# Performance work log

Measured on AMD Instinct MI355X. Metric: run time of the kernel, lower is better.

## Reference

```python
import jax, jax.numpy as jnp
import numpy as np

D_MODEL = 1024
NHEAD = 16
D_K = D_MODEL // NHEAD
BATCH = 8
SEQ = 1024
SPARSITY = 0.9


def setup_inputs() -> dict:
    key = jax.random.key(0)
    ks = jax.random.split(key, 13)
    q = jax.random.normal(ks[0], (BATCH, SEQ, D_MODEL), dtype=jnp.float32)
    k = jax.random.normal(ks[1], (BATCH, SEQ, D_MODEL), dtype=jnp.float32)
    v = jax.random.normal(ks[2], (BATCH, SEQ, D_MODEL), dtype=jnp.float32)
    mask = jax.random.uniform(ks[3], (BATCH, NHEAD, SEQ, SEQ)) > SPARSITY
    s = 1.0 / np.sqrt(D_MODEL)  # nn.Linear-style init scale
    def lin(kw, kb):
        W = jax.random.uniform(kw, (D_MODEL, D_MODEL), minval=-s, maxval=s, dtype=jnp.float32)
        b = jax.random.uniform(kb, (D_MODEL,), minval=-s, maxval=s, dtype=jnp.float32)
        return W, b
    Wq, bq = lin(ks[4], ks[5])
    Wk, bk = lin(ks[6], ks[7])
    Wv, bv = lin(ks[8], ks[9])
    Wo, bo = lin(ks[10], ks[11])
    return {"query": q, "key": k, "value": v, "mask": mask,
            "Wq": Wq, "bq": bq, "Wk": Wk, "bk": bk,
            "Wv": Wv, "bv": bv, "Wo": Wo, "bo": bo}


def reference(query, key, value, mask, Wq, bq, Wk, bk, Wv, bv, Wo, bo):
    B, S, _ = query.shape
    # projections (torch Linear: x @ W.T + b), split into heads -> [B, H, S, d_k]
    def proj(x, W, b):
        return (x @ W.T + b).reshape(B, S, NHEAD, D_K).transpose(0, 2, 1, 3)
    Q = proj(query, Wq, bq)
    K = proj(key, Wk, bk)
    V = proj(value, Wv, bv)
    scale = 1.0 / jnp.sqrt(jnp.float32(D_K))
    scores = jnp.einsum('bhqd,bhkd->bhqk', Q, K) * scale  # [B,H,S,S]
    scores = jnp.where(mask, scores, -jnp.inf)
    attn = jax.nn.softmax(scores, axis=-1)
    out = jnp.einsum('bhqk,bhkd->bhqd', attn, V)           # [B,H,S,d_k]
    out = out.transpose(0, 2, 1, 3).reshape(B, S, D_MODEL)
    return out @ Wo.T + bo
```

## Files before the change

### kernel.cpp

```cpp
#include <hip/hip_runtime.h>

typedef __bf16 bf16;
typedef bf16 bf16x4 __attribute__((ext_vector_type(4)));
typedef bf16 bf16x8 __attribute__((ext_vector_type(8)));
typedef float f32x4 __attribute__((ext_vector_type(4)));

#define D_MODEL 1024
#define NHEAD   16
#define D_K     64
#define BATCH   8
#define SEQL    1024
#define MROWS   (BATCH*SEQL)

struct Cvt7 {
    const float* s[7];
    bf16*        d[7];
    int          n[7];
};

__global__ __launch_bounds__(256) void cvt7_kernel(Cvt7 a) {
    const int y = blockIdx.y;
    const float* __restrict__ src = a.s[y];
    bf16* __restrict__ dst = a.d[y];
    const int n4 = a.n[y] >> 2;
    const int stride = gridDim.x * blockDim.x;
    for (int i = blockIdx.x * blockDim.x + threadIdx.x; i < n4; i += stride) {
        float4 v = ((const float4*)src)[i];
        bf16x4 o = { (bf16)v.x, (bf16)v.y, (bf16)v.z, (bf16)v.w };
        ((bf16x4*)dst)[i] = o;
    }
}

#define BM 128
#define BN 128
#define BK 32

__device__ __forceinline__ void gemm_core(const bf16* __restrict__ A, const bf16* __restrict__ B,
                                          int bm, int bn, int K,
                                          bf16* lA, bf16* lB, f32x4 (&acc)[4][4]) {
    const int t = threadIdx.x;
    const int lane = t & 63, w = t >> 6;
    const int wr = w >> 1, wc = w & 1;
    const int r = lane & 15, kb = lane >> 4;

    for (int k0 = 0; k0 < K; k0 += BK) {
        __syncthreads();
        #pragma unroll
        for (int i = 0; i < 2; ++i) {
            const int off = i * 4096 + w * 1024 + lane * 16;
            const int row = off >> 6;
            const int cb  = off & 63;
            const bf16* srcA = A + (size_t)(bm + row) * K + k0 + (cb >> 1);
            const bf16* srcB = B + (size_t)(bn + row) * K + k0 + (cb >> 1);
            __builtin_amdgcn_global_load_lds(
                (const __attribute__((address_space(1))) unsigned int*)srcA,
                (__attribute__((address_space(3))) unsigned int*)((char*)lA + i * 4096 + w * 1024),
                16, 0, 0);
            __builtin_amdgcn_global_load_lds(
                (const __attribute__((address_space(1))) unsigned int*)srcB,
                (__attribute__((address_space(3))) unsigned int*)((char*)lB + i * 4096 + w * 1024),
                16, 0, 0);
        }
        __syncthreads();

        bf16x8 af[4], bfr[4];
        #pragma unroll
        for (int m = 0; m < 4; ++m)
            af[m] = *(const bf16x8*)(lA + (wr * 64 + m * 16 + r) * BK + kb * 8);
        #pragma unroll
        for (int n = 0; n < 4; ++n)
            bfr[n] = *(const bf16x8*)(lB + (wc * 64 + n * 16 + r) * BK + kb * 8);
        #pragma unroll
        for (int m = 0; m < 4; ++m)
            #pragma unroll
            for (int n = 0; n < 4; ++n)
                acc[m][n] = __builtin_amdgcn_mfma_f32_16x16x32_bf16(af[m], bfr[n], acc[m][n], 0, 0, 0);
    }
}

__global__ __launch_bounds__(256) void proj3_kernel(
        const bf16* __restrict__ xq, const bf16* __restrict__ xk, const bf16* __restrict__ xv,
        const bf16* __restrict__ Wqb, const bf16* __restrict__ Wkb, const bf16* __restrict__ Wvb,
        const float* __restrict__ bq, const float* __restrict__ bk, const float* __restrict__ bv,
        bf16* __restrict__ Qp, bf16* __restrict__ Kp, bf16* __restrict__ Vt) {
    __shared__ bf16 lA[BM * BK], lB[BN * BK];
    const int z = blockIdx.z;
    const bf16* A    = (z == 0) ? xq  : (z == 1) ? xk  : xv;
    const bf16* Bm   = (z == 0) ? Wqb : (z == 1) ? Wkb : Wvb;
    const float* bias = (z == 0) ? bq : (z == 1) ? bk  : bv;
    const int bm = blockIdx.x * BM, bn = blockIdx.y * BN;

    f32x4 acc[4][4] = {};
    gemm_core(A, Bm, bm, bn, D_MODEL, lA, lB, acc);

    const int lane = threadIdx.x & 63, w = threadIdx.x >> 6;
    const int wr = w >> 1, wc = w & 1, r = lane & 15, g = lane >> 4;
    #pragma unroll
    for (int n = 0; n < 4; ++n) {
        const int col = bn + wc * 64 + n * 16 + r;
        const float bvl = bias[col];
        const int h = col >> 6, d = col & 63;
        #pragma unroll
        for (int m = 0; m < 4; ++m) {
            #pragma unroll
            for (int j = 0; j < 4; ++j) {
                const int row = bm + wr * 64 + m * 16 + g * 4 + j;
                const float v = acc[m][n][j] + bvl;
                const int b = row >> 10, s = row & (SEQL - 1);
                const int bh = b * NHEAD + h;
                if (z == 0) {
                    Qp[((size_t)bh * SEQL + s) * D_K + d] = (bf16)v;
                } else if (z == 1) {
                    Kp[((size_t)bh * SEQL + s) * D_K + d] = (bf16)v;
                } else {
                    Vt[((size_t)bh * D_K + d) * SEQL + s] = (bf16)v;
                }
            }
        }
    }
}

__global__ __launch_bounds__(256) void outproj_kernel(
        const bf16* __restrict__ AO, const bf16* __restrict__ Wob,
        const float* __restrict__ bo, float* __restrict__ out) {
    __shared__ bf16 lA[BM * BK], lB[BN * BK];
    const int bm = blockIdx.x * BM, bn = blockIdx.y * BN;
    f32x4 acc[4][4] = {};
    gemm_core(AO, Wob, bm, bn, D_MODEL, lA, lB, acc);

    const int lane = threadIdx.x & 63, w = threadIdx.x >> 6;
    const int wr = w >> 1, wc = w & 1, r = lane & 15, g = lane >> 4;
    #pragma unroll
    for (int n = 0; n < 4; ++n) {
        const int col = bn + wc * 64 + n * 16 + r;
        const float bvl = bo[col];
        #pragma unroll
        for (int m = 0; m < 4; ++m)
            #pragma unroll
            for (int j = 0; j < 4; ++j) {
                const int row = bm + wr * 64 + m * 16 + g * 4 + j;
                out[(size_t)row * D_MODEL + col] = acc[m][n][j] + bvl;
            }
    }
}

__global__ __launch_bounds__(256, 4) void attn_kernel(
        const bf16* __restrict__ Qp, const bf16* __restrict__ Kp, const bf16* __restrict__ Vt,
        const unsigned int* __restrict__ mask, bf16* __restrict__ AO) {
    __shared__ char kbuf[8192];
    __shared__ char vbuf[8192];
    __shared__ char mbuf[16384];
    __shared__ bf16 plds[4][16 * 64];
    const int lin = blockIdx.x + blockIdx.y * gridDim.x;
    const int xcd = lin & 7, pos = lin >> 3;
    const int bh  = xcd * 16 + (pos >> 4);
    const int qt  = pos & 15;
    const int b = bh >> 4, h = bh & 15;
    const int t = threadIdx.x, lane = t & 63, w = t >> 6;
    const int q0 = qt * 64;
    const int r = lane & 15, g = lane >> 4;

    const char* __restrict__ Kb = (const char*)(Kp + (size_t)bh * SEQL * D_K);
    const char* __restrict__ Vb = (const char*)(Vt + (size_t)bh * D_K * SEQL);
    const char* __restrict__ Mb = (const char*)(mask + ((size_t)bh * SEQL + q0) * SEQL);

    const bf16* __restrict__ Qh = Qp + ((size_t)bh * SEQL + q0 + w * 16) * D_K;
    bf16x8 qf[2];
    #pragma unroll
    for (int kk = 0; kk < 2; ++kk)
        qf[kk] = *(const bf16x8*)(Qh + r * D_K + kk * 32 + g * 8);

    f32x4 o[4] = {};
    float psum = 0.f;
    char* P = (char*)plds[w];
    const int swz = (r & 7) << 4;

    for (int s0 = 0; s0 < SEQL; s0 += 64) {
        __syncthreads();
        #pragma unroll
        for (int i = 0; i < 2; ++i) {
            const int slot = i * 256 + t;
            const int row = slot >> 3, ch = slot & 7;
            const char* srcK = Kb + (size_t)(s0 + row) * 128 + ((ch * 16) ^ ((row & 7) << 4));
            const char* srcV = Vb + (size_t)row * (SEQL * 2) + s0 * 2 + ((ch * 16) ^ ((row & 7) << 4));
            __builtin_amdgcn_global_load_lds(
                (const __attribute__((address_space(1))) unsigned int*)srcK,
                (__attribute__((address_space(3))) unsigned int*)(kbuf + i * 4096 + w * 1024),
                16, 0, 0);
            __builtin_amdgcn_global_load_lds(
                (const __attribute__((address_space(1))) unsigned int*)srcV,
                (__attribute__((address_space(3))) unsigned int*)(vbuf + i * 4096 + w * 1024),
                16, 0, 0);
        }
        #pragma unroll
        for (int i = 0; i < 4; ++i) {
            const int slot = i * 256 + t;
            const int row = slot >> 4, ch = slot & 15;
            const char* srcM = Mb + (size_t)row * (SEQL * 4) + s0 * 4 + ((ch * 16) ^ ((row & 7) << 4));
            __builtin_amdgcn_global_load_lds(
                (const __attribute__((address_space(1))) unsigned int*)srcM,
                (__attribute__((address_space(3))) unsigned int*)(mbuf + i * 4096 + w * 1024),
                16, 0, 0);
        }
        __syncthreads();

        f32x4 sf[4] = {};
        __builtin_amdgcn_s_setprio(1);
        #pragma unroll
        for (int n = 0; n < 4; ++n) {
            #pragma unroll
            for (int kk = 0; kk < 2; ++kk) {
                const int krow = n * 16 + r;
                bf16x8 kf = *(const bf16x8*)(kbuf + krow * 128 + ((kk * 64 + g * 16) ^ swz));
                sf[n] = __builtin_amdgcn_mfma_f32_16x16x32_bf16(kf, qf[kk], sf[n], 0, 0, 0);
            }
        }
        __builtin_amdgcn_s_setprio(0);
        const int mrow = w * 16 + r;
        #pragma unroll
        for (int n = 0; n < 4; ++n) {
            const uint4 mv = *(const uint4*)(mbuf + mrow * 256 + ((n * 64 + g * 16) ^ swz));
            const float p0 = mv.x ? __expf(sf[n][0] * 0.125f) : 0.f;
            const float p1 = mv.y ? __expf(sf[n][1] * 0.125f) : 0.f;
            const float p2 = mv.z ? __expf(sf[n][2] * 0.125f) : 0.f;
            const float p3 = mv.w ? __expf(sf[n][3] * 0.125f) : 0.f;
            psum += (p0 + p1) + (p2 + p3);
            bf16x4 pb = { (bf16)p0, (bf16)p1, (bf16)p2, (bf16)p3 };
            *(bf16x4*)(P + ((r * 128 + n * 32 + g * 8) ^ swz)) = pb;
        }
        bf16x8 pf0 = *(const bf16x8*)(P + ((r * 128 + 0 * 64 + g * 16) ^ swz));
        bf16x8 pf1 = *(const bf16x8*)(P + ((r * 128 + 1 * 64 + g * 16) ^ swz));
        __builtin_amdgcn_s_setprio(1);
        #pragma unroll
        for (int n = 0; n < 4; ++n) {
            const int vrow = n * 16 + r;
            bf16x8 vf0 = *(const bf16x8*)(vbuf + vrow * 128 + ((0 * 64 + g * 16) ^ swz));
            bf16x8 vf1 = *(const bf16x8*)(vbuf + vrow * 128 + ((1 * 64 + g * 16) ^ swz));
            o[n] = __builtin_amdgcn_mfma_f32_16x16x32_bf16(vf0, pf0, o[n], 0, 0, 0);
            o[n] = __builtin_amdgcn_mfma_f32_16x16x32_bf16(vf1, pf1, o[n], 0, 0, 0);
        }
        __builtin_amdgcn_s_setprio(0);
    }

    psum += __shfl_xor(psum, 16);
    psum += __shfl_xor(psum, 32);
    const float inv = 1.0f / psum;

    const size_t rowbase = ((size_t)(b * SEQL + q0 + w * 16 + r)) * D_MODEL + h * D_K;
    #pragma unroll
    for (int n = 0; n < 4; ++n) {
        bf16x4 ob = { (bf16)(o[n][0] * inv), (bf16)(o[n][1] * inv),
                      (bf16)(o[n][2] * inv), (bf16)(o[n][3] * inv) };
        *(bf16x4*)(AO + rowbase + n * 16 + g * 4) = ob;
    }
}

extern "C" void kernel_launch(void* const* d_in, const int* in_sizes, int n_in,
                              void* d_out, int out_size, void* d_ws, size_t ws_size,
                              hipStream_t stream) {
    const float* q    = (const float*)d_in[0];
    const float* k    = (const float*)d_in[1];
    const float* v    = (const float*)d_in[2];
    const unsigned int* mask = (const unsigned int*)d_in[3];
    const float* Wq = (const float*)d_in[4];
    const float* bq = (const float*)d_in[5];
    const float* Wk = (const float*)d_in[6];
    const float* bk = (const float*)d_in[7];
    const float* Wv = (const float*)d_in[8];
    const float* bv = (const float*)d_in[9];
    const float* Wo = (const float*)d_in[10];
    const float* bo = (const float*)d_in[11];

    char* ws = (char*)d_ws;
    const size_t MB = 1u << 20;
    bf16* qb  = (bf16*)(ws + 0 * MB);
    bf16* kb  = (bf16*)(ws + 16 * MB);
    bf16* vb  = (bf16*)(ws + 32 * MB);
    bf16* Wqb = (bf16*)(ws + 48 * MB);
    bf16* Wkb = (bf16*)(ws + 50 * MB);
    bf16* Wvb = (bf16*)(ws + 52 * MB);
    bf16* Wob = (bf16*)(ws + 54 * MB);
    bf16* Qp  = (bf16*)(ws + 56 * MB);
    bf16* Kp  = (bf16*)(ws + 72 * MB);
    bf16* Vt  = (bf16*)(ws + 88 * MB);
    bf16* AO  = (bf16*)(ws + 104 * MB);

    Cvt7 c;
    c.s[0] = q;  c.d[0] = qb;  c.n[0] = MROWS * D_MODEL;
    c.s[1] = k;  c.d[1] = kb;  c.n[1] = MROWS * D_MODEL;
    c.s[2] = v;  c.d[2] = vb;  c.n[2] = MROWS * D_MODEL;
    c.s[3] = Wq; c.d[3] = Wqb; c.n[3] = D_MODEL * D_MODEL;
    c.s[4] = Wk; c.d[4] = Wkb; c.n[4] = D_MODEL * D_MODEL;
    c.s[5] = Wv; c.d[5] = Wvb; c.n[5] = D_MODEL * D_MODEL;
    c.s[6] = Wo; c.d[6] = Wob; c.n[6] = D_MODEL * D_MODEL;
    cvt7_kernel<<<dim3(1024, 7), 256, 0, stream>>>(c);

    proj3_kernel<<<dim3(MROWS / BM, D_MODEL / BN, 3), 256, 0, stream>>>(
        qb, kb, vb, Wqb, Wkb, Wvb, bq, bk, bv, Qp, Kp, Vt);

    attn_kernel<<<dim3(SEQL / 64, BATCH * NHEAD), 256, 0, stream>>>(Qp, Kp, Vt, mask, AO);

    outproj_kernel<<<dim3(MROWS / BM, D_MODEL / BN), 256, 0, stream>>>(AO, Wob, bo, (float*)d_out);
}
```

Measured before the change: 292.1 us.

## Pack mask into bitmask concurrently with projections; read bits in attention

Adds a mask-packing path that turns the 32-bit-per-element mask into 64-bit ballot bitmasks. It runs in every fourth block of the merged projection kernel, so it overlaps with the Q/K/V GEMMs. The attention kernel then loads each tile's packed mask bits once into LDS, instead of streaming the full uint mask per key tile, which cuts its mask traffic by a large factor. The full mask is still read once during packing, and the packed mask is stored temporarily in the output buffer before outproj overwrites it.

```diff
diff --git a/kernel.cpp b/kernel.cpp
--- a/kernel.cpp
+++ b/kernel.cpp
@@ -11,6 +11,7 @@
 #define BATCH   8
 #define SEQL    1024
 #define MROWS   (BATCH*SEQL)
+#define MWORDS  ((size_t)BATCH*NHEAD*SEQL*SEQL)
 
 struct Cvt7 {
     const float* s[7];
@@ -78,17 +79,41 @@
     }
 }
 
-__global__ __launch_bounds__(256) void proj3_kernel(
+__global__ __launch_bounds__(256) void projpack_kernel(
         const bf16* __restrict__ xq, const bf16* __restrict__ xk, const bf16* __restrict__ xv,
         const bf16* __restrict__ Wqb, const bf16* __restrict__ Wkb, const bf16* __restrict__ Wvb,
         const float* __restrict__ bq, const float* __restrict__ bk, const float* __restrict__ bv,
+        const unsigned int* __restrict__ mask, unsigned long long* __restrict__ Mp,
         bf16* __restrict__ Qp, bf16* __restrict__ Kp, bf16* __restrict__ Vt) {
     __shared__ bf16 lA[BM * BK], lB[BN * BK];
-    const int z = blockIdx.z;
+    const int bid = blockIdx.x;
+
+    if ((bid & 3) == 3) {
+        const int lane = threadIdx.x & 63;
+        const int wid  = (((bid >> 2) * 256 + threadIdx.x) >> 6);
+        const size_t ngrp = MWORDS / 256;
+        for (size_t i = wid; i < ngrp; i += 2048) {
+            const unsigned int* base = mask + i * 256;
+            const unsigned long long o0 = __ballot(base[0 * 64 + lane] != 0);
+            const unsigned long long o1 = __ballot(base[1 * 64 + lane] != 0);
+            const unsigned long long o2 = __ballot(base[2 * 64 + lane] != 0);
+            const unsigned long long o3 = __ballot(base[3 * 64 + lane] != 0);
+            if (lane < 4) {
+                const unsigned long long v = lane == 0 ? o0 : lane == 1 ? o1 : lane == 2 ? o2 : o3;
+                Mp[i * 4 + lane] = v;
+            }
+        }
+        return;
+    }
+
+    const int projIdx = (bid >> 2) * 3 + (bid & 3);
+    const int z   = projIdx / 512;
+    const int rem = projIdx % 512;
+    const int bm = (rem & 63) * BM;
+    const int bn = (rem >> 6) * BN;
     const bf16* A    = (z == 0) ? xq  : (z == 1) ? xk  : xv;
     const bf16* Bm   = (z == 0) ? Wqb : (z == 1) ? Wkb : Wvb;
     const float* bias = (z == 0) ? bq : (z == 1) ? bk  : bv;
-    const int bm = blockIdx.x * BM, bn = blockIdx.y * BN;
 
     f32x4 acc[4][4] = {};
     gemm_core(A, Bm, bm, bn, D_MODEL, lA, lB, acc);
@@ -146,11 +171,11 @@
 
 __global__ __launch_bounds__(256, 4) void attn_kernel(
         const bf16* __restrict__ Qp, const bf16* __restrict__ Kp, const bf16* __restrict__ Vt,
-        const unsigned int* __restrict__ mask, bf16* __restrict__ AO) {
+        const unsigned long long* __restrict__ Mp, bf16* __restrict__ AO) {
     __shared__ char kbuf[8192];
     __shared__ char vbuf[8192];
-    __shared__ char mbuf[16384];
     __shared__ bf16 plds[4][16 * 64];
+    __shared__ unsigned long long mbits[64][16];
     const int lin = blockIdx.x + blockIdx.y * gridDim.x;
     const int xcd = lin & 7, pos = lin >> 3;
     const int bh  = xcd * 16 + (pos >> 4);
@@ -162,7 +187,14 @@
 
     const char* __restrict__ Kb = (const char*)(Kp + (size_t)bh * SEQL * D_K);
     const char* __restrict__ Vb = (const char*)(Vt + (size_t)bh * D_K * SEQL);
-    const char* __restrict__ Mb = (const char*)(mask + ((size_t)bh * SEQL + q0) * SEQL);
+
+    const char* Mpb = (const char*)(Mp + ((size_t)bh * SEQL + q0) * 16);
+    __builtin_amdgcn_global_load_lds(
+        (const __attribute__((address_space(1))) unsigned int*)(Mpb + t * 16),
+        (__attribute__((address_space(3))) unsigned int*)((char*)mbits + t * 16), 16, 0, 0);
+    __builtin_amdgcn_global_load_lds(
+        (const __attribute__((address_space(1))) unsigned int*)(Mpb + 4096 + t * 16),
+        (__attribute__((address_space(3))) unsigned int*)((char*)mbits + 4096 + t * 16), 16, 0, 0);
 
     const bf16* __restrict__ Qh = Qp + ((size_t)bh * SEQL + q0 + w * 16) * D_K;
     bf16x8 qf[2];
@@ -192,16 +224,6 @@
                 (__attribute__((address_space(3))) unsigned int*)(vbuf + i * 4096 + w * 1024),
                 16, 0, 0);
         }
-        #pragma unroll
-        for (int i = 0; i < 4; ++i) {
-            const int slot = i * 256 + t;
-            const int row = slot >> 4, ch = slot & 15;
-            const char* srcM = Mb + (size_t)row * (SEQL * 4) + s0 * 4 + ((ch * 16) ^ ((row & 7) << 4));
-            __builtin_amdgcn_global_load_lds(
-                (const __attribute__((address_space(1))) unsigned int*)srcM,
-                (__attribute__((address_space(3))) unsigned int*)(mbuf + i * 4096 + w * 1024),
-                16, 0, 0);
-        }
         __syncthreads();
 
         f32x4 sf[4] = {};
@@ -216,14 +238,13 @@
             }
         }
         __builtin_amdgcn_s_setprio(0);
-        const int mrow = w * 16 + r;
+        const unsigned long long sh = mbits[w * 16 + r][s0 >> 6] >> (g * 4);
         #pragma unroll
         for (int n = 0; n < 4; ++n) {
-            const uint4 mv = *(const uint4*)(mbuf + mrow * 256 + ((n * 64 + g * 16) ^ swz));
-            const float p0 = mv.x ? __expf(sf[n][0] * 0.125f) : 0.f;
-            const float p1 = mv.y ? __expf(sf[n][1] * 0.125f) : 0.f;
-            const float p2 = mv.z ? __expf(sf[n][2] * 0.125f) : 0.f;
-            const float p3 = mv.w ? __expf(sf[n][3] * 0.125f) : 0.f;
+            const float p0 = ((sh >> (n * 16 + 0)) & 1ull) ? __expf(sf[n][0] * 0.125f) : 0.f;
+            const float p1 = ((sh >> (n * 16 + 1)) & 1ull) ? __expf(sf[n][1] * 0.125f) : 0.f;
+            const float p2 = ((sh >> (n * 16 + 2)) & 1ull) ? __expf(sf[n][2] * 0.125f) : 0.f;
+            const float p3 = ((sh >> (n * 16 + 3)) & 1ull) ? __expf(sf[n][3] * 0.125f) : 0.f;
             psum += (p0 + p1) + (p2 + p3);
             bf16x4 pb = { (bf16)p0, (bf16)p1, (bf16)p2, (bf16)p3 };
             *(bf16x4*)(P + ((r * 128 + n * 32 + g * 8) ^ swz)) = pb;
@@ -284,6 +305,7 @@
     bf16* Kp  = (bf16*)(ws + 72 * MB);
     bf16* Vt  = (bf16*)(ws + 88 * MB);
     bf16* AO  = (bf16*)(ws + 104 * MB);
+    unsigned long long* Mp = (unsigned long long*)d_out;
 
     Cvt7 c;
     c.s[0] = q;  c.d[0] = qb;  c.n[0] = MROWS * D_MODEL;
@@ -295,10 +317,10 @@
     c.s[6] = Wo; c.d[6] = Wob; c.n[6] = D_MODEL * D_MODEL;
     cvt7_kernel<<<dim3(1024, 7), 256, 0, stream>>>(c);
 
-    proj3_kernel<<<dim3(MROWS / BM, D_MODEL / BN, 3), 256, 0, stream>>>(
-        qb, kb, vb, Wqb, Wkb, Wvb, bq, bk, bv, Qp, Kp, Vt);
-
-    attn_kernel<<<dim3(SEQL / 64, BATCH * NHEAD), 256, 0, stream>>>(Qp, Kp, Vt, mask, AO);
+    projpack_kernel<<<2048, 256, 0, stream>>>(
+        qb, kb, vb, Wqb, Wkb, Wvb, bq, bk, bv, mask, Mp, Qp, Kp, Vt);
+
+    attn_kernel<<<dim3(SEQL / 64, BATCH * NHEAD), 256, 0, stream>>>(Qp, Kp, Vt, Mp, AO);
 
     outproj_kernel<<<dim3(MROWS / BM, D_MODEL / BN), 256, 0, stream>>>(AO, Wob, bo, (float*)d_out);
 }
```

After: 596.1 us. 2.04x slower.
